# Kernel tuning notes

Hardware: AMD Instinct MI355X
Metric: run time of the kernel (lower is better)

## Reference

```python
import jax, jax.numpy as jnp
import numpy as np

NUM_HEADS = 8


def setup_inputs() -> dict:
    key = jax.random.key(0)
    k1, k2 = jax.random.split(key)
    B, N, C = 2, 8192, 512
    x = jax.random.normal(k1, (B, N, C), dtype=jnp.float32)
    # torch nn.Linear weight layout: [out_features, in_features]
    W_qkv = jax.random.normal(k2, (3 * C, C), dtype=jnp.float32) * (C ** -0.5)
    return {"x": x, "W_qkv": W_qkv}


def reference(x, W_qkv):
    B, N, C = x.shape
    H = NUM_HEADS
    d = C // H
    scale = d ** -0.5

    # qkv projection (no bias): [B, N, 3C]
    qkv = x @ W_qkv.T
    # [B, N, 3, H, d] -> [3, B, H, N, d]
    qkv = qkv.reshape(B, N, 3, H, d).transpose(2, 0, 3, 1, 4)
    q, k, v = qkv[0], qkv[1], qkv[2]

    # mean-center keys over sequence dim
    k_hat = k - jnp.mean(k, axis=2, keepdims=True)          # [B, H, N, d]

    # KV aggregation: g = k_hat^T @ v  -> [B, H, d, d]
    g = jnp.einsum('bhnd,bhne->bhde', k_hat, v)

    # k_sum over sequence (numerically ~0 since k_hat is centered, kept faithful)
    k_sum = jnp.sum(k_hat, axis=2)                          # [B, H, d]
    q_ksum = jnp.einsum('bhnd,bhd->bhn', q, k_sum)[..., None]  # [B, H, N, 1]

    # denominator: N*scale + q @ k_sum^T
    t_D = N * scale + q_ksum                                # [B, H, N, 1]
    # numerator: scale + q @ g (broadcast of ones*scale over last dim)
    T_N = scale + jnp.einsum('bhnd,bhde->bhne', q, g)       # [B, H, N, d]

    z = T_N / t_D                                           # [B, H, N, d]
    return z
```

## Files before the change

kernel.cpp:

```cpp
#include <hip/hip_runtime.h>

typedef unsigned short u16;
typedef unsigned int u32;
typedef __attribute__((ext_vector_type(8))) short short8;
typedef __attribute__((ext_vector_type(4))) float f32x4;
typedef __attribute__((ext_vector_type(4))) unsigned short ushort4v;
typedef __attribute__((ext_vector_type(4))) float float4v;

__device__ __forceinline__ float bf2f(u16 u) {
    return __uint_as_float(((u32)u) << 16);
}
__device__ __forceinline__ u16 f2bf(float f) {
    u32 u = __float_as_uint(f);
    u += 0x7FFF + ((u >> 16) & 1);
    return (u16)(u >> 16);
}
__device__ __forceinline__ short8 cvt8(float4 a, float4 b) {
    short8 r;
    r[0] = (short)f2bf(a.x); r[1] = (short)f2bf(a.y);
    r[2] = (short)f2bf(a.z); r[3] = (short)f2bf(a.w);
    r[4] = (short)f2bf(b.x); r[5] = (short)f2bf(b.y);
    r[6] = (short)f2bf(b.z); r[7] = (short)f2bf(b.w);
    return r;
}
__device__ __forceinline__ void stage16(const u16* g, u16* l) {
    __builtin_amdgcn_global_load_lds(
        (const __attribute__((address_space(1))) unsigned int*)g,
        (__attribute__((address_space(3))) unsigned int*)l, 16, 0, 0);
}

__global__ __launch_bounds__(256) void cvt_t(const float* __restrict__ x,
                                             u16* __restrict__ xT,
                                             u16* __restrict__ xb,
                                             float* __restrict__ sp2,
                                             const float* __restrict__ W,
                                             u16* __restrict__ wvb,
                                             u16* __restrict__ Ub) {
    __shared__ __align__(16) char smem[36864];
    const int bid = blockIdx.x;
    const int t = threadIdx.x;
    if (bid >= 1280) {
        const int u = bid - 1280;
        const int h = u >> 4, mt = (u >> 2) & 3, ntt = u & 3;
        u16 (*At)[72] = (u16(*)[72])smem;
        u16 (*Bt)[72] = (u16(*)[72])(smem + 18432);
        const int d = t >> 2, cg = (t & 3) * 32;
        const float* wq = W + (size_t)(h * 64 + d) * 512 + mt * 128 + cg;
        const float* wk = W + (size_t)(512 + h * 64 + d) * 512 + ntt * 128 + cg;
#pragma unroll
        for (int j = 0; j < 32; j += 4) {
            float4 a = *(const float4*)(wq + j);
            float4 kk = *(const float4*)(wk + j);
            At[cg + j + 0][d] = f2bf(a.x); At[cg + j + 1][d] = f2bf(a.y);
            At[cg + j + 2][d] = f2bf(a.z); At[cg + j + 3][d] = f2bf(a.w);
            Bt[cg + j + 0][d] = f2bf(kk.x); Bt[cg + j + 1][d] = f2bf(kk.y);
            Bt[cg + j + 2][d] = f2bf(kk.z); Bt[cg + j + 3][d] = f2bf(kk.w);
        }
        __syncthreads();
        const int l = t & 63, wv = t >> 6;
        const int lr = l & 15, lk = (l >> 4) * 8;
        const int wm = (wv >> 1) * 64, wn = (wv & 1) * 64;
        f32x4 zz = {0.f, 0.f, 0.f, 0.f};
        f32x4 acc[4][4];
        for (int i = 0; i < 4; ++i)
            for (int j = 0; j < 4; ++j) acc[i][j] = zz;
#pragma unroll
        for (int k0 = 0; k0 < 64; k0 += 32) {
            short8 af[4], bfr[4];
#pragma unroll
            for (int mi = 0; mi < 4; ++mi)
                af[mi] = *(const short8*)(&At[wm + mi * 16 + lr][k0 + lk]);
#pragma unroll
            for (int ni = 0; ni < 4; ++ni)
                bfr[ni] = *(const short8*)(&Bt[wn + ni * 16 + lr][k0 + lk]);
#pragma unroll
            for (int mi = 0; mi < 4; ++mi)
#pragma unroll
                for (int ni = 0; ni < 4; ++ni)
                    acc[mi][ni] = __builtin_amdgcn_mfma_f32_16x16x32_bf16(
                        af[mi], bfr[ni], acc[mi][ni], 0, 0, 0);
        }
#pragma unroll
        for (int mi = 0; mi < 4; ++mi)
#pragma unroll
            for (int ni = 0; ni < 4; ++ni) {
                int col = ntt * 128 + wn + ni * 16 + lr;
#pragma unroll
                for (int j = 0; j < 4; ++j) {
                    int row = mt * 128 + wm + mi * 16 + (l >> 4) * 4 + j;
                    Ub[((size_t)(h * 512 + row)) * 512 + col] = f2bf(acc[mi][ni][j]);
                }
            }
        return;
    }
    if (bid >= 1024) {
        const int i = (bid - 1024) * 256 + t;
        float4v v = ((const float4v*)(W + 524288))[i];
        ushort4v r;
        r[0] = f2bf(v[0]); r[1] = f2bf(v[1]); r[2] = f2bf(v[2]); r[3] = f2bf(v[3]);
        ((ushort4v*)wvb)[i] = r;
        return;
    }
    u16 (*tile)[136] = (u16(*)[136])smem;
    const int ct = bid & 3, nt = (bid >> 2) & 127, b = bid >> 9;
    const int r = t >> 2, c0 = (t & 3) * 32;
    const float* src = x + ((size_t)(b * 8192 + nt * 64 + r)) * 512 + ct * 128 + c0;
    short8 r8[4];
#pragma unroll
    for (int j = 0; j < 8; j += 2) {
        float4 v0 = *(const float4*)(src + j * 4);
        float4 v1 = *(const float4*)(src + j * 4 + 4);
        r8[j >> 1] = cvt8(v0, v1);
        *(short8*)(&tile[r][c0 + j * 4]) = r8[j >> 1];
    }
    u16* xbrow = xb + ((size_t)(b * 8192 + nt * 64 + r)) * 512 + ct * 128 + c0;
#pragma unroll
    for (int jj = 0; jj < 4; ++jj) *(short8*)(xbrow + jj * 8) = r8[jj];
    __syncthreads();
    const int c = t >> 1, half = t & 1;
    u16 vals[32];
    float psum = 0.f;
#pragma unroll
    for (int i = 0; i < 32; ++i) {
        vals[i] = tile[half * 32 + i][c];
        psum += bf2f(vals[i]);
    }
    u16* dst = xT + ((size_t)(b * 512 + ct * 128 + c)) * 8192 + nt * 64 + half * 32;
#pragma unroll
    for (int j = 0; j < 4; ++j)
        *(int4*)(dst + j * 8) = *(int4*)(&vals[j * 8]);
    psum += __shfl_xor(psum, 1);
    if ((t & 1) == 0)
        sp2[((size_t)(b * 128 + nt)) * 512 + ct * 128 + c] = psum;
}

template <int STRIDE, int KLEN>
__device__ __forceinline__ void gemm_core(const u16* __restrict__ Ag,
                                          const u16* __restrict__ Bg,
                                          u16* As, u16* Bs, int t,
                                          f32x4 acc[4][4]) {
    const int wv = t >> 6, l = t & 63;
    const int lr = l & 15, lk = (l >> 4) * 8;
    const int wm = (wv >> 1) * 64, wn = (wv & 1) * 64;
    const int srow = l >> 2, scol = (l & 3) * 8;

    u16* Ad0 = As + (wv * 32) * 32;
    u16* Ad1 = As + (wv * 32 + 16) * 32;
    u16* Bd0 = Bs + (wv * 32) * 32;
    u16* Bd1 = Bs + (wv * 32 + 16) * 32;
    const u16* As0 = Ag + (size_t)(wv * 32 + srow) * STRIDE + scol;
    const u16* As1 = Ag + (size_t)(wv * 32 + 16 + srow) * STRIDE + scol;
    const u16* Bs0 = Bg + (size_t)(wv * 32 + srow) * STRIDE + scol;
    const u16* Bs1 = Bg + (size_t)(wv * 32 + 16 + srow) * STRIDE + scol;

    for (int k0 = 0; k0 < KLEN; k0 += 32) {
        stage16(As0 + k0, Ad0);
        stage16(As1 + k0, Ad1);
        stage16(Bs0 + k0, Bd0);
        stage16(Bs1 + k0, Bd1);
        __syncthreads();
        short8 af[4], bfr[4];
#pragma unroll
        for (int mi = 0; mi < 4; ++mi)
            af[mi] = *(const short8*)(As + (wm + mi * 16 + lr) * 32 + lk);
#pragma unroll
        for (int ni = 0; ni < 4; ++ni)
            bfr[ni] = *(const short8*)(Bs + (wn + ni * 16 + lr) * 32 + lk);
#pragma unroll
        for (int mi = 0; mi < 4; ++mi)
#pragma unroll
            for (int ni = 0; ni < 4; ++ni)
                acc[mi][ni] = __builtin_amdgcn_mfma_f32_16x16x32_bf16(
                    af[mi], bfr[ni], acc[mi][ni], 0, 0, 0);
        __syncthreads();
    }
}

__global__ __launch_bounds__(256) void syrk(const u16* __restrict__ xT,
                                            u16* __restrict__ Spart,
                                            const float* __restrict__ sp2,
                                            float* __restrict__ ssum) {
    const int bid = blockIdx.x, t = threadIdx.x;
    if (bid >= 512) {
        const int idx = (bid - 512) * 256 + t;
        const int b = idx >> 9, c = idx & 511;
        float a = 0.f;
        for (int j = 0; j < 128; ++j) a += sp2[(size_t)(b * 128 + j) * 512 + c];
        ssum[idx] = a;
        return;
    }
    const int wid = (bid & 7) * 64 + (bid >> 3);
    __shared__ u16 As[128 * 32];
    __shared__ u16 Bs[128 * 32];
    const int nt = wid & 3, mt = (wid >> 2) & 3;
    const int ks = (wid >> 4) & 15, b = wid >> 8;
    const u16* Ag = xT + ((size_t)(b * 512 + mt * 128)) * 8192 + ks * 512;
    const u16* Bg = xT + ((size_t)(b * 512 + nt * 128)) * 8192 + ks * 512;

    f32x4 zz = {0.f, 0.f, 0.f, 0.f};
    f32x4 acc[4][4];
    for (int i = 0; i < 4; ++i)
        for (int j = 0; j < 4; ++j) acc[i][j] = zz;

    gemm_core<8192, 512>(Ag, Bg, As, Bs, t, acc);

    const int l = t & 63, wv = t >> 6;
    const int lr = l & 15;
    const int wm = (wv >> 1) * 64, wn = (wv & 1) * 64;
    u16* out = Spart + ((size_t)(b * 16 + ks)) * 262144;
#pragma unroll
    for (int mi = 0; mi < 4; ++mi)
#pragma unroll
        for (int ni = 0; ni < 4; ++ni) {
            int col = nt * 128 + wn + ni * 16 + lr;
#pragma unroll
            for (int j = 0; j < 4; ++j) {
                int row = mt * 128 + wm + mi * 16 + (l >> 4) * 4 + j;
                out[(size_t)row * 512 + col] = f2bf(acc[mi][ni][j]);
            }
        }
}

__global__ __launch_bounds__(256) void reduceS(const u16* __restrict__ Spart,
                                               const float* __restrict__ s,
                                               u16* __restrict__ Sbf) {
    const int b = blockIdx.x >> 9, m = blockIdx.x & 511;
    const int t = threadIdx.x;
    const float sm = s[b * 512 + m] * (1.0f / 8192.0f);
    const int n0 = t * 2;
    float a0 = 0.f, a1 = 0.f;
#pragma unroll
    for (int ks = 0; ks < 16; ++ks) {
        u32 v = *(const u32*)(Spart + ((size_t)(b * 16 + ks)) * 262144 +
                              (size_t)m * 512 + n0);
        a0 += bf2f((u16)(v & 0xffff));
        a1 += bf2f((u16)(v >> 16));
    }
    a0 -= sm * s[b * 512 + n0];
    a1 -= sm * s[b * 512 + n0 + 1];
    u32 packed = (u32)f2bf(a0) | ((u32)f2bf(a1) << 16);
    *(u32*)(Sbf + (size_t)b * 262144 + (size_t)m * 512 + n0) = packed;
}

__global__ __launch_bounds__(256) void pgemm(const u16* __restrict__ wvb,
                                             const u16* __restrict__ Sbf,
                                             float* __restrict__ Ppart) {
    __shared__ u16 As[128 * 32];
    __shared__ u16 Bs[128 * 32];
    const int t = threadIdx.x;
    const int nt = blockIdx.x & 3, mt = (blockIdx.x >> 2) & 3;
    const int ks = (blockIdx.x >> 4) & 3, b = blockIdx.x >> 6;
    const u16* Ag = wvb + (size_t)(mt * 128) * 512 + ks * 128;
    const u16* Bg = Sbf + (size_t)b * 262144 + (size_t)(nt * 128) * 512 + ks * 128;

    f32x4 zz = {0.f, 0.f, 0.f, 0.f};
    f32x4 acc[4][4];
    for (int i = 0; i < 4; ++i)
        for (int j = 0; j < 4; ++j) acc[i][j] = zz;

    gemm_core<512, 128>(Ag, Bg, As, Bs, t, acc);

    const int l = t & 63, wv = t >> 6;
    const int lr = l & 15;
    const int wm = (wv >> 1) * 64, wn = (wv & 1) * 64;
    float* out = Ppart + ((size_t)(b * 4 + ks)) * 262144;
#pragma unroll
    for (int mi = 0; mi < 4; ++mi)
#pragma unroll
        for (int ni = 0; ni < 4; ++ni) {
            int col = nt * 128 + wn + ni * 16 + lr;
#pragma unroll
            for (int j = 0; j < 4; ++j) {
                int row = mt * 128 + wm + mi * 16 + (l >> 4) * 4 + j;
                out[(size_t)row * 512 + col] = acc[mi][ni][j];
            }
        }
}

__global__ __launch_bounds__(256) void wgg(const u16* __restrict__ Ub,
                                           const float* __restrict__ Ppart,
                                           float* __restrict__ Wgpart) {
    __shared__ u16 As[64 * 136];
    __shared__ u16 Bs[128 * 32];
    const int ks = blockIdx.x & 3, ct = (blockIdx.x >> 2) & 3, bh = blockIdx.x >> 4;
    const int b = bh >> 3, h = bh & 7;
    const int t = threadIdx.x, wv = t >> 6, l = t & 63;
    const int lr = l & 15, lk = (l >> 4) * 8;
    const int wm = (wv >> 1) * 32, wn = (wv & 1) * 64;
    const int srow = l >> 2, scol = (l & 3) * 8;

    const float* Pb0 = Ppart + ((size_t)(b * 4)) * 262144 +
                       ((size_t)(h * 64)) * 512 + ks * 128;
#pragma unroll
    for (int i = 0; i < 8; ++i) {
        int idx = i * 1024 + t * 4;
        int r = idx >> 7, c = idx & 127;
        const float* p = Pb0 + (size_t)r * 512 + c;
        float4 s0 = *(const float4*)(p);
        float4 s1 = *(const float4*)(p + 262144);
        float4 s2 = *(const float4*)(p + 524288);
        float4 s3 = *(const float4*)(p + 786432);
        ushort4v r4v;
        r4v[0] = f2bf(s0.x + s1.x + s2.x + s3.x);
        r4v[1] = f2bf(s0.y + s1.y + s2.y + s3.y);
        r4v[2] = f2bf(s0.z + s1.z + s2.z + s3.z);
        r4v[3] = f2bf(s0.w + s1.w + s2.w + s3.w);
        *(ushort4v*)(&As[r * 136 + c]) = r4v;
    }

    const u16* Bg = Ub + (size_t)(h * 512 + ct * 128) * 512 + ks * 128;
    u16* Bd0 = Bs + (wv * 32) * 32;
    u16* Bd1 = Bs + (wv * 32 + 16) * 32;
    const u16* Bs0 = Bg + (size_t)(wv * 32 + srow) * 512 + scol;
    const u16* Bs1 = Bg + (size_t)(wv * 32 + 16 + srow) * 512 + scol;

    f32x4 zz = {0.f, 0.f, 0.f, 0.f};
    f32x4 acc[2][4];
    for (int i = 0; i < 2; ++i)
        for (int j = 0; j < 4; ++j) acc[i][j] = zz;

    __syncthreads();
    for (int k0 = 0; k0 < 128; k0 += 32) {
        stage16(Bs0 + k0, Bd0);
        stage16(Bs1 + k0, Bd1);
        __syncthreads();
        short8 af[2], bfr[4];
#pragma unroll
        for (int mi = 0; mi < 2; ++mi)
            af[mi] = *(const short8*)(As + (wm + mi * 16 + lr) * 136 + k0 + lk);
#pragma unroll
        for (int ni = 0; ni < 4; ++ni)
            bfr[ni] = *(const short8*)(Bs + (wn + ni * 16 + lr) * 32 + lk);
#pragma unroll
        for (int mi = 0; mi < 2; ++mi)
#pragma unroll
            for (int ni = 0; ni < 4; ++ni)
                acc[mi][ni] = __builtin_amdgcn_mfma_f32_16x16x32_bf16(
                    af[mi], bfr[ni], acc[mi][ni], 0, 0, 0);
        __syncthreads();
    }
#pragma unroll
    for (int mi = 0; mi < 2; ++mi)
#pragma unroll
        for (int ni = 0; ni < 4; ++ni) {
            int col = ct * 128 + wn + ni * 16 + lr;
#pragma unroll
            for (int j = 0; j < 4; ++j) {
                int row = wm + mi * 16 + (l >> 4) * 4 + j;
                Wgpart[((size_t)(ks * 1024 + b * 512 + h * 64 + row)) * 512 + col] =
                    acc[mi][ni][j];
            }
        }
}

__global__ __launch_bounds__(256) void reduceW(const float* __restrict__ Wgpart,
                                               u16* __restrict__ Wgb) {
    int idx = blockIdx.x * 1024 + threadIdx.x;
    for (int r = 0; r < 4; ++r, idx += 256) {
        float acc = 0.f;
#pragma unroll
        for (int ks = 0; ks < 4; ++ks)
            acc += Wgpart[(size_t)ks * 524288 + idx];
        Wgb[idx] = f2bf(acc);
    }
}

__global__ __launch_bounds__(256) void out_z(const u16* __restrict__ xb,
                                             const u16* __restrict__ Wgb,
                                             float* __restrict__ z) {
    __shared__ u16 As[128 * 32];
    __shared__ u16 Bs[128 * 32];
    const int t = threadIdx.x;
    const int m0 = blockIdx.x * 128;
    const int b = blockIdx.x >> 6;
    const int n0 = blockIdx.y * 128;

    f32x4 zz = {0.f, 0.f, 0.f, 0.f};
    f32x4 acc[4][4];
    for (int i = 0; i < 4; ++i)
        for (int j = 0; j < 4; ++j) acc[i][j] = zz;

    gemm_core<512, 512>(xb + (size_t)m0 * 512,
                        Wgb + (size_t)b * 262144 + (size_t)n0 * 512, As, Bs, t, acc);

    const int l = t & 63, wv = t >> 6;
    const int lr = l & 15;
    const int wm = (wv >> 1) * 64, wn = (wv & 1) * 64;
#pragma unroll
    for (int mi = 0; mi < 4; ++mi)
#pragma unroll
        for (int ni = 0; ni < 4; ++ni) {
            int he = n0 + wn + ni * 16 + lr;
            int h = he >> 6, e = he & 63;
#pragma unroll
            for (int j = 0; j < 4; ++j) {
                int row = m0 + wm + mi * 16 + (l >> 4) * 4 + j;
                int nidx = row & 8191;
                z[((size_t)(b * 8 + h) * 8192 + nidx) * 64 + e] =
                    (acc[mi][ni][j] + 0.125f) * 0.0009765625f;
            }
        }
}

extern "C" void kernel_launch(void* const* d_in, const int* in_sizes, int n_in,
                              void* d_out, int out_size, void* d_ws, size_t ws_size,
                              hipStream_t stream) {
    const float* x = (const float*)d_in[0];
    const float* W = (const float*)d_in[1];
    float* z = (float*)d_out;

    char* ws = (char*)d_ws;
    u16* xT       = (u16*)(ws);
    u16* xb       = (u16*)(ws + 16777216);
    u16* Spart    = (u16*)(ws + 33554432);
    u16* Sbf      = (u16*)(ws + 50331648);
    float* sp2    = (float*)(ws + 51380224);
    float* ssum   = (float*)(ws + 51904512);
    u16* wvb      = (u16*)(ws + 51908608);
    u16* Ub       = (u16*)(ws + 53481472);
    u16* Wgb      = (u16*)(ws + 57675776);
    float* Ppart  = (float*)(ws + 58724352);
    float* Wgpart = (float*)(ws + 67112960);

    cvt_t<<<1408, 256, 0, stream>>>(x, xT, xb, sp2, W, wvb, Ub);
    syrk<<<516, 256, 0, stream>>>(xT, Spart, sp2, ssum);
    reduceS<<<1024, 256, 0, stream>>>(Spart, ssum, Sbf);
    pgemm<<<128, 256, 0, stream>>>(wvb, Sbf, Ppart);
    wgg<<<256, 256, 0, stream>>>(Ub, Ppart, Wgpart);
    reduceW<<<512, 256, 0, stream>>>(Wgpart, Wgb);
    out_z<<<dim3(128, 4), 256, 0, stream>>>(xb, Wgb, z);
}
```

Baseline: 77.79 us.

## Exploit Gram matrix symmetry in syrk by computing only upper-triangular tiles

The syrk kernel computes the x^T x partial Gram matrices. It now launches only the 10 upper-triangular 128x128 tile pairs per k-split instead of all 16. For off-diagonal tiles it transposes the accumulator through a padded shared-memory buffer and also writes the mirrored tile with vectorized stores. This removes about 40% of the MFMA and load work, at the cost of extra shared-memory traffic, syncs and a second store for off-diagonal tiles.

```diff
diff --git a/kernel.cpp b/kernel.cpp
--- a/kernel.cpp
+++ b/kernel.cpp
@@ -181,19 +181,26 @@
                                             const float* __restrict__ sp2,
                                             float* __restrict__ ssum) {
     const int bid = blockIdx.x, t = threadIdx.x;
-    if (bid >= 512) {
-        const int idx = (bid - 512) * 256 + t;
+    if (bid >= 320) {
+        const int idx = (bid - 320) * 256 + t;
         const int b = idx >> 9, c = idx & 511;
         float a = 0.f;
         for (int j = 0; j < 128; ++j) a += sp2[(size_t)(b * 128 + j) * 512 + c];
         ssum[idx] = a;
         return;
     }
-    const int wid = (bid & 7) * 64 + (bid >> 3);
+    const int wid = (bid & 7) * 40 + (bid >> 3);
+    const int p = wid % 10;
+    const int ks = (wid / 10) & 15, b = wid / 160;
+    int mt, nt;
+    if (p < 4)      { mt = 0; nt = p; }
+    else if (p < 7) { mt = 1; nt = p - 3; }
+    else if (p < 9) { mt = 2; nt = p - 5; }
+    else            { mt = 3; nt = 3; }
+
     __shared__ u16 As[128 * 32];
     __shared__ u16 Bs[128 * 32];
-    const int nt = wid & 3, mt = (wid >> 2) & 3;
-    const int ks = (wid >> 4) & 15, b = wid >> 8;
+    __shared__ u16 Ts[64][136];
     const u16* Ag = xT + ((size_t)(b * 512 + mt * 128)) * 8192 + ks * 512;
     const u16* Bg = xT + ((size_t)(b * 512 + nt * 128)) * 8192 + ks * 512;
 
@@ -219,6 +226,31 @@
                 out[(size_t)row * 512 + col] = f2bf(acc[mi][ni][j]);
             }
         }
+
+    if (mt != nt) {
+#pragma unroll
+        for (int ch = 0; ch < 2; ++ch) {
+            __syncthreads();
+            if ((wv >> 1) == ch) {
+#pragma unroll
+                for (int mi = 0; mi < 4; ++mi)
+#pragma unroll
+                    for (int ni = 0; ni < 4; ++ni)
+#pragma unroll
+                        for (int j = 0; j < 4; ++j)
+                            Ts[mi * 16 + (l >> 4) * 4 + j][wn + ni * 16 + lr] =
+                                f2bf(acc[mi][ni][j]);
+            }
+            __syncthreads();
+            const int n = t >> 1, mh = (t & 1) * 32;
+            u16 buf[32];
+#pragma unroll
+            for (int i = 0; i < 32; ++i) buf[i] = Ts[mh + i][n];
+            u16* d = out + (size_t)(nt * 128 + n) * 512 + mt * 128 + ch * 64 + mh;
+#pragma unroll
+            for (int q = 0; q < 4; ++q) *(int4*)(d + q * 8) = *(const int4*)(&buf[q * 8]);
+        }
+    }
 }
 
 __global__ __launch_bounds__(256) void reduceS(const u16* __restrict__ Spart,
@@ -423,7 +455,7 @@
     float* Wgpart = (float*)(ws + 67112960);
 
     cvt_t<<<1408, 256, 0, stream>>>(x, xT, xb, sp2, W, wvb, Ub);
-    syrk<<<516, 256, 0, stream>>>(xT, Spart, sp2, ssum);
+    syrk<<<324, 256, 0, stream>>>(xT, Spart, sp2, ssum);
     reduceS<<<1024, 256, 0, stream>>>(Spart, ssum, Sbf);
     pgemm<<<128, 256, 0, stream>>>(wvb, Sbf, Ppart);
     wgg<<<256, 256, 0, stream>>>(Ub, Ppart, Wgpart);
```

Result: slower. 80.28 us (+3.2%).
